# Kernel tuning notes

Measured on AMD Instinct MI355X. Metric: run time of the kernel, lower is better.

Reference implementation:

```python
import jax, jax.numpy as jnp
import numpy as np

DIM, HEADS, DH, M, PINV_ITERS, RES_K = 512, 8, 64, 256, 6, 33

def layernorm(x, w, b, eps=1e-5):
    mu = jnp.mean(x, -1, keepdims=True)
    var = jnp.var(x, -1, keepdims=True)
    return (x - mu) * jax.lax.rsqrt(var + eps) * w + b

def pinv_iter(x, iters=PINV_ITERS):
    # Moore-Penrose iterative pseudo-inverse (lucidrains nystrom-attention)
    ax = jnp.abs(x)
    z = jnp.swapaxes(x, -1, -2) / (jnp.max(ax.sum(-1)) * jnp.max(ax.sum(-2)))
    I = jnp.eye(x.shape[-1], dtype=x.dtype)
    for _ in range(iters):
        xz = x @ z
        z = 0.25 * z @ (13 * I - xz @ (15 * I - xz @ (7 * I - xz)))
    return z

def _core(x, w_qkv):
    b, n, _ = x.shape
    pad = (M - n % M) % M            # Nystrom pads at the FRONT to a multiple of m=256
    xp = jnp.pad(x, ((0, 0), (pad, 0), (0, 0)))
    npad = n + pad
    q, k, v = jnp.split(xp @ w_qkv, 3, axis=-1)
    split_heads = lambda t: t.reshape(b, npad, HEADS, DH).transpose(0, 2, 1, 3)
    q = split_heads(q) * (DH ** -0.5)
    k, v = split_heads(k), split_heads(v)
    l = npad // M                    # tokens per landmark
    q_l = q.reshape(b, HEADS, M, l, DH).mean(3)
    k_l = k.reshape(b, HEADS, M, l, DH).mean(3)
    return q, k, v, q_l, k_l, pad, n

def nystrom_out(x, w_qkv, w_out, b_out, res_kernel):
    q, k, v, q_l, k_l, pad, n = _core(x, w_qkv)
    attn1 = jax.nn.softmax(jnp.einsum('bhid,bhjd->bhij', q, k_l), -1)    # (b,h,N,M)
    attn2 = jax.nn.softmax(jnp.einsum('bhid,bhjd->bhij', q_l, k_l), -1)  # (b,h,M,M)
    attn3 = jax.nn.softmax(jnp.einsum('bhid,bhjd->bhij', q_l, k), -1)    # (b,h,M,N)
    out = (attn1 @ pinv_iter(attn2)) @ (attn3 @ v)
    # depthwise residual conv over sequence dim, per head
    out = out + jax.lax.conv_general_dilated(
        v, res_kernel, (1, 1), [(RES_K // 2, RES_K // 2), (0, 0)],
        dimension_numbers=('NCHW', 'OIHW', 'NCHW'), feature_group_count=HEADS)
    b = out.shape[0]
    out = out.transpose(0, 2, 1, 3).reshape(b, -1, HEADS * DH) @ w_out + b_out
    return out[:, -n:]

def nystrom_cls_row(x, w_qkv):
    # cls-token (query index pad, head 0) row of attn1 @ pinv(attn2) @ attn3;
    # identical math to the full (n x n) matrix row the torch code slices out.
    q, k, v, q_l, k_l, pad, n = _core(x, w_qkv)
    q0, k0, ql0, kl0 = q[:, 0], k[:, 0], q_l[:, 0], k_l[:, 0]
    attn2 = jax.nn.softmax(ql0 @ jnp.swapaxes(kl0, -1, -2), -1)   # (b,M,M)
    attn3 = jax.nn.softmax(ql0 @ jnp.swapaxes(k0, -1, -2), -1)    # (b,M,N)
    row1 = jax.nn.softmax(jnp.einsum('bd,bjd->bj', q0[:, pad], kl0), -1)
    row = jnp.einsum('bj,bjk->bk', row1, pinv_iter(attn2))
    row = jnp.einsum('bk,bkn->bn', row, attn3)                    # (b, N_padded)
    return row, pad

def dwconv(x, k, b, p):
    y = jax.lax.conv_general_dilated(x, k, (1, 1), [(p, p), (p, p)],
        dimension_numbers=('NCHW', 'OIHW', 'NCHW'), feature_group_count=x.shape[1])
    return y + b[None, :, None, None]

def leff(x, k7, b7, k5, b5, k3, b3, Hs, Ws):
    cls_t, feat = x[:, :1], x[:, 1:]
    B, N, C = feat.shape
    img = feat.transpose(0, 2, 1).reshape(B, C, Hs, Ws)
    y = dwconv(img, k7, b7, 3) + img + dwconv(img, k5, b5, 2) + dwconv(img, k3, b3, 1)
    y = y.reshape(B, C, Hs * Ws).transpose(0, 2, 1)
    return jnp.concatenate([cls_t, y], axis=1)

def setup_inputs():
    key = jax.random.key(0)
    ks = iter(jax.random.split(key, 32))
    n, n_classes = 22500, 2
    p = {}
    p['h'] = jax.random.normal(next(ks), (n, 1024), jnp.float32)
    p['fc1_w'] = jax.random.normal(next(ks), (1024, DIM), jnp.float32) * 0.02
    p['fc1_b'] = jnp.zeros((DIM,), jnp.float32)
    p['cls_token'] = jax.random.normal(next(ks), (1, 1, DIM), jnp.float32)
    for pre in ('l1', 'l2'):
        p[pre + '_ln_w'] = jnp.ones((DIM,), jnp.float32)
        p[pre + '_ln_b'] = jnp.zeros((DIM,), jnp.float32)
        p[pre + '_wqkv'] = jax.random.normal(next(ks), (DIM, 3 * HEADS * DH), jnp.float32) * 0.02
        p[pre + '_wout'] = jax.random.normal(next(ks), (HEADS * DH, DIM), jnp.float32) * 0.02
        p[pre + '_bout'] = jnp.zeros((DIM,), jnp.float32)
        p[pre + '_resk'] = jax.random.normal(next(ks), (HEADS, 1, RES_K, 1), jnp.float32) * 0.05
    for kk in (7, 5, 3):
        p['leff_k%d' % kk] = jax.random.normal(next(ks), (DIM, 1, kk, kk), jnp.float32) * 0.05
        p['leff_b%d' % kk] = jnp.zeros((DIM,), jnp.float32)
    p['norm_w'] = jnp.ones((DIM,), jnp.float32)
    p['norm_b'] = jnp.zeros((DIM,), jnp.float32)
    p['fc2_w'] = jax.random.normal(next(ks), (DIM, n_classes), jnp.float32) * 0.02
    p['fc2_b'] = jnp.zeros((n_classes,), jnp.float32)
    return p

def reference(h, fc1_w, fc1_b, cls_token,
              l1_ln_w, l1_ln_b, l1_wqkv, l1_wout, l1_bout, l1_resk,
              leff_k7, leff_b7, leff_k5, leff_b5, leff_k3, leff_b3,
              l2_ln_w, l2_ln_b, l2_wqkv, l2_wout, l2_bout, l2_resk,
              norm_w, norm_b, fc2_w, fc2_b):
    x = h[None]                                   # (1, n, 1024)
    n = x.shape[1]
    x = jax.nn.relu(x @ fc1_w + fc1_b)            # (1, n, 512)
    Hs = int(np.ceil(np.sqrt(n)))                 # 150 for n=22500
    add_len = Hs * Hs - n
    if add_len > 0:
        x = jnp.concatenate([x, x[:, :add_len]], axis=1)
    x = jnp.concatenate([jnp.broadcast_to(cls_token, (1, 1, DIM)), x], axis=1)
    # TransLayer 1
    x = x + nystrom_out(layernorm(x, l1_ln_w, l1_ln_b), l1_wqkv, l1_wout, l1_bout, l1_resk)
    # LeFF positional layer
    x = leff(x, leff_k7, leff_b7, leff_k5, leff_b5, leff_k3, leff_b3, Hs, Hs)
    # TransLayer 2 (first call in TransMIL.forward)
    h2 = x + nystrom_out(layernorm(x, l2_ln_w, l2_ln_b), l2_wqkv, l2_wout, l2_bout, l2_resk)
    # TransLayer 2 second call: residual update then attention matrix of updated state
    h3 = h2 + nystrom_out(layernorm(h2, l2_ln_w, l2_ln_b), l2_wqkv, l2_wout, l2_bout, l2_resk)
    row, pad = nystrom_cls_row(layernorm(h3, l2_ln_w, l2_ln_b), l2_wqkv)
    A = row[0, pad + 1: pad + 1 + n][:, None]     # (n, 1) cls->instance attention
    hf = layernorm(h2, norm_w, norm_b)[:, 0]      # (1, 512)
    logits = hf @ fc2_w + fc2_b                   # (1, n_classes)
    Y_prob = jax.nn.softmax(logits, -1)
    return logits, Y_prob, A
```

## Files before the change

kernel.cpp:

```cpp
#include <hip/hip_runtime.h>

#define NTOK 22500
#define N1   22501
#define NPAD 22528
#define PADR 27
#define DIM  512
#define NH   8
#define DHD  64
#define MM   256
#define LLM  88
#define HSZ  150
#define CSZ  256
#define NCH  88

typedef short bf16x8 __attribute__((ext_vector_type(8)));
typedef float f32x4  __attribute__((ext_vector_type(4)));
typedef unsigned short us;

union U8 { bf16x8 v; unsigned short u[8]; };

__device__ __forceinline__ unsigned short f2b(float f){
  unsigned int u = __float_as_uint(f);
  unsigned int r = u + 0x7fffu + ((u>>16)&1u);
  return (unsigned short)(r>>16);
}
__device__ __forceinline__ float bf2f(unsigned short u){
  return __uint_as_float(((unsigned int)u)<<16);
}
__device__ __forceinline__ bf16x8 cvt8(float4 a, float4 b){
  U8 u;
  u.u[0]=f2b(a.x); u.u[1]=f2b(a.y); u.u[2]=f2b(a.z); u.u[3]=f2b(a.w);
  u.u[4]=f2b(b.x); u.u[5]=f2b(b.y); u.u[6]=f2b(b.z); u.u[7]=f2b(b.w);
  return u.v;
}
__device__ __forceinline__ void gld16(const void* g, void* l){
  __builtin_amdgcn_global_load_lds(
      (const __attribute__((address_space(1))) void*)g,
      (__attribute__((address_space(3))) void*)l, 16, 0, 0);
}

__device__ __forceinline__ float waveSum(float v){
#pragma unroll
  for (int o=32;o>0;o>>=1) v += __shfl_down(v,o);
  return v;
}
__device__ __forceinline__ float waveMax(float v){
#pragma unroll
  for (int o=32;o>0;o>>=1) v = fmaxf(v,__shfl_down(v,o));
  return v;
}
__device__ __forceinline__ float blockSum256(float v, float* sb){
  v = waveSum(v);
  __syncthreads();
  if ((threadIdx.x&63)==0) sb[threadIdx.x>>6]=v;
  __syncthreads();
  return sb[0]+sb[1]+sb[2]+sb[3];
}
__device__ __forceinline__ float blockMax256(float v, float* sb){
  v = waveMax(v);
  __syncthreads();
  if ((threadIdx.x&63)==0) sb[threadIdx.x>>6]=v;
  __syncthreads();
  return fmaxf(fmaxf(sb[0],sb[1]),fmaxf(sb[2],sb[3]));
}

__global__ void k_wT(const float* __restrict__ W, us* __restrict__ Bt, int K, int N)
{
  __shared__ float tile[32][33];
  int tx = threadIdx.x&31, ty = threadIdx.x>>5;
  int k0 = blockIdx.x*32, n0 = blockIdx.y*32;
#pragma unroll
  for (int i=0;i<4;++i){
    int k = k0+ty+i*8;
    if (k<K && n0+tx<N) tile[ty+i*8][tx] = W[(size_t)k*N + n0+tx];
  }
  __syncthreads();
#pragma unroll
  for (int i=0;i<4;++i){
    int n = n0+ty+i*8, k = k0+tx;
    if (n<N && k<K) Bt[(size_t)n*K + k] = f2b(tile[tx][ty+i*8]);
  }
}

__global__ void k_vT(const us* __restrict__ V, us* __restrict__ Vt)
{
  __shared__ us tile[32][33];
  int tx = threadIdx.x&31, ty = threadIdx.x>>5;
  int p0 = blockIdx.x*32;
  int h = blockIdx.y>>1, d0 = (blockIdx.y&1)*32;
#pragma unroll
  for (int i=0;i<4;++i){
    int p = p0+ty+i*8;
    tile[ty+i*8][tx] = V[((size_t)h*NPAD+p)*DHD + d0+tx];
  }
  __syncthreads();
#pragma unroll
  for (int i=0;i<4;++i){
    int d = d0+ty+i*8;
    Vt[((size_t)h*DHD+d)*NPAD + p0+tx] = tile[tx][ty+i*8];
  }
}

template<int MODE, int BM>
__global__ __launch_bounds__(256) void k_gemm(const float* __restrict__ Af,
    const us* __restrict__ Ab, const us* __restrict__ Bt, const float* __restrict__ bias,
    us* __restrict__ Xb, float* __restrict__ Cf, float* __restrict__ C2,
    us* __restrict__ Q_, us* __restrict__ K_, us* __restrict__ V_,
    const us* __restrict__ zpg, int Kd, int ntn)
{
  __shared__ us SM[BM*64 + 128*64];
  us* As = SM;
  us* Bs = SM + BM*64;
  const int tid = threadIdx.x;
  const int bid = blockIdx.x;
  const int ntile = bid % ntn;
  const int m0 = (bid / ntn)*BM, n0 = ntile*128;
  const int lane = tid & 63;
  const int wid = tid >> 6;
  constexpr int MT = BM/32;
  constexpr int ACH = BM/32;
  const int wm = (wid>>1)*(BM/2), wn = (wid&1)*64;
  f32x4 acc[MT][4] = {};
  for (int k0=0; k0<Kd; k0+=64){
    __syncthreads();
    if (MODE==0){
#pragma unroll
      for (int i=0;i<BM/16;++i){
        int g = i*256 + tid;
        int row = g>>4, k4 = (g&15)*4;
        int gm = m0 + row;
        ushort4 h4 = make_ushort4(0,0,0,0);
        if (gm < NTOK){
          float4 v = *(const float4*)(Af + (size_t)gm*Kd + k0 + k4);
          h4.x=f2b(v.x); h4.y=f2b(v.y); h4.z=f2b(v.z); h4.w=f2b(v.w);
        }
        *(ushort4*)(&As[row*64 + (k4 ^ ((row&7)<<3))]) = h4;
      }
    } else {
#pragma unroll
      for (int i=0;i<ACH;++i){
        int c = wid*ACH+i;
        int row = c*8 + (lane>>3);
        int scol8 = ((lane&7) ^ (row&7))*8;
        int gm = m0+row;
        const us* ga;
        if (MODE==2) ga = Ab + ((size_t)((gm<N1?gm:0)+PADR))*Kd + k0 + scol8;
        else ga = (gm>=PADR) ? Ab + (size_t)(gm-PADR)*Kd + k0 + scol8 : zpg + scol8;
        gld16(ga, &As[c*512]);
      }
    }
#pragma unroll
    for (int i=0;i<4;++i){
      int c = wid*4+i;
      int row = c*8 + (lane>>3);
      int scol8 = ((lane&7) ^ (row&7))*8;
      int vn = n0+row;
      if (MODE==3) vn = (vn<64)? vn : vn+448;
      gld16(Bt + (size_t)vn*Kd + k0 + scol8, &Bs[c*512]);
    }
    __syncthreads();
#pragma unroll
    for (int ks=0; ks<2; ++ks){
      const int kk = ks*32 + (lane>>4)*8;
      bf16x8 af[MT], bfm[4];
#pragma unroll
      for (int t=0;t<MT;++t){
        int r = wm + t*16 + (lane&15);
        af[t] = *(bf16x8*)(&As[r*64 + (kk ^ ((r&7)<<3))]);
      }
#pragma unroll
      for (int t=0;t<4;++t){
        int c = wn + t*16 + (lane&15);
        bfm[t] = *(bf16x8*)(&Bs[c*64 + (kk ^ ((c&7)<<3))]);
      }
#pragma unroll
      for (int mt=0;mt<MT;++mt)
#pragma unroll
        for (int nt=0;nt<4;++nt)
          acc[mt][nt] = __builtin_amdgcn_mfma_f32_16x16x32_bf16(af[mt], bfm[nt], acc[mt][nt], 0,0,0);
    }
  }
  const int rbase = (lane>>4)*4;
  const int cl = lane&15;
  if (MODE==3){
#pragma unroll
    for (int mt=0;mt<MT;++mt)
#pragma unroll
      for (int r=0;r<4;++r){
        int gm = m0 + wm + mt*16 + rbase + r;
#pragma unroll
        for (int nt=0;nt<4;++nt){
          int gn = n0 + wn + nt*16 + cl;
          float v = acc[mt][nt][r];
          if (gn < 64) Cf[(size_t)gm*DHD + gn] = v*0.125f;
          else         C2[(size_t)gm*DHD + (gn-64)] = v;
        }
      }
    return;
  }
  const float sc1 = (MODE==1 && (ntile>>2)==0) ? 0.125f : 1.f;
  __syncthreads();
#pragma unroll
  for (int mt=0;mt<MT;++mt)
#pragma unroll
    for (int r=0;r<4;++r){
      int row = wm + mt*16 + rbase + r;
#pragma unroll
      for (int nt=0;nt<4;++nt){
        int col = wn + nt*16 + cl;
        float v = acc[mt][nt][r];
        if (MODE==0){ v += bias[n0+col]; v = v>0.f?v:0.f; }
        else if (MODE==2){ v += bias[n0+col]; }
        else v *= sc1;
        SM[row*128 + col] = f2b(v);
      }
    }
  __syncthreads();
  if (MODE==1){
    const int sec = ntile>>2;
    us* dst = sec==0 ? Q_ : (sec==1 ? K_ : V_);
#pragma unroll
    for (int i=0;i<BM/16;++i){
      int v8 = i*256 + tid;
      int row = v8>>4, c8 = (v8&15)*8;
      int gm = m0 + row, gn = n0 + c8;
      int hh = (gn>>6)&7, d = gn&63;
      *(bf16x8*)(dst + ((size_t)hh*NPAD+gm)*DHD + d) = *(bf16x8*)(&SM[row*128 + c8]);
    }
  } else if (MODE==0){
#pragma unroll
    for (int i=0;i<BM/16;++i){
      int v8 = i*256 + tid;
      int row = v8>>4, c8 = (v8&15)*8;
      int gm = m0 + row;
      if (gm < NTOK)
        *(bf16x8*)(Xb + (size_t)(1+gm)*DIM + n0 + c8) = *(bf16x8*)(&SM[row*128 + c8]);
    }
  } else {
#pragma unroll
    for (int i=0;i<BM/16;++i){
      int v8 = i*256 + tid;
      int row = v8>>4, c8 = (v8&15)*8;
      int gm = m0 + row;
      if (gm < N1){
        us* p = Xb + (size_t)gm*DIM + n0 + c8;
        U8 xo, ad, o;
        xo.v = *(bf16x8*)p;
        ad.v = *(bf16x8*)(&SM[row*128 + c8]);
#pragma unroll
        for (int j=0;j<8;++j) o.u[j] = f2b(bf2f(xo.u[j]) + bf2f(ad.u[j]));
        *(bf16x8*)p = o.v;
      }
    }
  }
}

__global__ void k_setcls(us* __restrict__ X, const float* __restrict__ cls){
  int i = blockIdx.x*256 + threadIdx.x;
  if (i < DIM) X[i] = f2b(cls[i]);
}
__global__ void k_copyu(us* __restrict__ d, const us* __restrict__ s, size_t n){
  size_t i = (size_t)blockIdx.x*256 + threadIdx.x;
  if (i<n) d[i]=s[i];
}

__global__ void k_ln(const us* __restrict__ X, us* __restrict__ Y,
                     const float* __restrict__ w, const float* __restrict__ b)
{
  __shared__ float sb[4];
  const us* x = X + (size_t)blockIdx.x*DIM;
  us* y = Y + (size_t)blockIdx.x*DIM;
  int t = threadIdx.x;
  ushort2 xv = *(const ushort2*)(x + 2*t);
  float a0=bf2f(xv.x), a1=bf2f(xv.y);
  float s = blockSum256(a0+a1, sb);
  float q = blockSum256(a0*a0+a1*a1, sb);
  float mean = s*(1.f/512.f);
  float var = q*(1.f/512.f) - mean*mean;
  float rstd = rsqrtf(var+1e-5f);
  float2 wv = *(const float2*)(w + 2*t);
  float2 bv = *(const float2*)(b + 2*t);
  ushort2 o;
  o.x = f2b((a0-mean)*rstd*wv.x+bv.x);
  o.y = f2b((a1-mean)*rstd*wv.y+bv.y);
  *(ushort2*)(y + 2*t) = o;
}

__global__ void k_landmark2(const us* __restrict__ Q, const us* __restrict__ K,
                            us* __restrict__ QL, us* __restrict__ KL)
{
  int hm = blockIdx.x;
  bool isK = hm >= NH*MM;
  if (isK) hm -= NH*MM;
  int h = hm>>8, m = hm&255; int d = threadIdx.x;
  const us* base = (isK?K:Q) + ((size_t)h*NPAD + (size_t)m*LLM)*DHD + d;
  float s = 0.f;
  for (int j=0;j<LLM;++j) s += bf2f(base[(size_t)j*DHD]);
  (isK?KL:QL)[((size_t)h*MM + m)*DHD + d] = f2b(s * (1.f/(float)LLM));
}
__global__ void k_landmark2f(const float* __restrict__ Q, const float* __restrict__ K,
                             float* __restrict__ QL, float* __restrict__ KL)
{
  int hm = blockIdx.x;
  bool isK = hm >= MM;
  int m = isK ? hm-MM : hm; int d = threadIdx.x;
  const float* base = (isK?K:Q) + (size_t)m*LLM*DHD + d;
  float s = 0.f;
  for (int j=0;j<LLM;++j) s += base[(size_t)j*DHD];
  (isK?KL:QL)[(size_t)m*DHD + d] = s * (1.f/(float)LLM);
}

__global__ __launch_bounds__(64) void k_nt64(const float* __restrict__ A,
    const float* __restrict__ B, float* __restrict__ C,
    long sA, long sB, long sC, int Nr)
{
  int lane = threadIdx.x;
  int n0 = blockIdx.x*64, m0 = blockIdx.y*64;
  A += (size_t)blockIdx.z*sA; B += (size_t)blockIdx.z*sB; C += (size_t)blockIdx.z*sC;
  f32x4 acc[4][4] = {};
#pragma unroll
  for (int ks=0;ks<2;++ks){
    int kk = ks*32 + (lane>>4)*8;
    bf16x8 af[4], bfr[4];
#pragma unroll
    for (int mt=0;mt<4;++mt){
      const float* p = A + (size_t)(m0+mt*16+(lane&15))*64 + kk;
      af[mt] = cvt8(*(const float4*)p, *(const float4*)(p+4));
    }
#pragma unroll
    for (int nt=0;nt<4;++nt){
      const float* p = B + (size_t)(n0+nt*16+(lane&15))*64 + kk;
      bfr[nt] = cvt8(*(const float4*)p, *(const float4*)(p+4));
    }
#pragma unroll
    for (int mt=0;mt<4;++mt)
#pragma unroll
      for (int nt=0;nt<4;++nt)
        acc[mt][nt] = __builtin_amdgcn_mfma_f32_16x16x32_bf16(af[mt], bfr[nt], acc[mt][nt], 0,0,0);
  }
#pragma unroll
  for (int mt=0;mt<4;++mt)
#pragma unroll
    for (int r=0;r<4;++r){
      int row = m0+mt*16+(lane>>4)*4+r;
#pragma unroll
      for (int nt=0;nt<4;++nt){
        int col = n0+nt*16+(lane&15);
        C[(size_t)row*Nr + col] = acc[mt][nt][r];
      }
    }
}

__global__ __launch_bounds__(64) void k_nt64b(const us* __restrict__ A,
    const us* __restrict__ B, float* __restrict__ C,
    long sA, long sB, long sC, int Nr)
{
  int lane = threadIdx.x;
  int n0 = blockIdx.x*64, m0 = blockIdx.y*64;
  A += (size_t)blockIdx.z*sA; B += (size_t)blockIdx.z*sB; C += (size_t)blockIdx.z*sC;
  f32x4 acc[4][4] = {};
#pragma unroll
  for (int ks=0;ks<2;++ks){
    int kk = ks*32 + (lane>>4)*8;
    bf16x8 af[4], bfr[4];
#pragma unroll
    for (int mt=0;mt<4;++mt)
      af[mt] = *(const bf16x8*)(A + (size_t)(m0+mt*16+(lane&15))*64 + kk);
#pragma unroll
    for (int nt=0;nt<4;++nt)
      bfr[nt] = *(const bf16x8*)(B + (size_t)(n0+nt*16+(lane&15))*64 + kk);
#pragma unroll
    for (int mt=0;mt<4;++mt)
#pragma unroll
      for (int nt=0;nt<4;++nt)
        acc[mt][nt] = __builtin_amdgcn_mfma_f32_16x16x32_bf16(af[mt], bfr[nt], acc[mt][nt], 0,0,0);
  }
#pragma unroll
  for (int mt=0;mt<4;++mt)
#pragma unroll
    for (int r=0;r<4;++r){
      int row = m0+mt*16+(lane>>4)*4+r;
#pragma unroll
      for (int nt=0;nt<4;++nt){
        int col = n0+nt*16+(lane&15);
        C[(size_t)row*Nr + col] = acc[mt][nt][r];
      }
    }
}

template<int PM>
__global__ __launch_bounds__(256) void k_pgemm(const us* __restrict__ A,
    const us* __restrict__ Bt, us* __restrict__ C, us* __restrict__ Ct,
    float dc, float alpha, int writeC)
{
  __shared__ us As[64*256];
  __shared__ us Bs[64*256];
  const int tid = threadIdx.x, lane = tid&63, wid = tid>>6;
  const int n0 = blockIdx.x*64, m0 = blockIdx.y*64;
  const us* Ab = A + (size_t)blockIdx.z*65536;
  const us* Bb = Bt + (size_t)blockIdx.z*65536;
  for (int i=tid; i<4096; i+=256){
    int r = i>>6, c4 = (i&63)*4;
    *(ushort4*)(&As[r*256 + (c4 ^ ((r&7)<<3))]) = *(const ushort4*)(Ab + (size_t)(m0+r)*256 + c4);
    *(ushort4*)(&Bs[r*256 + (c4 ^ ((r&7)<<3))]) = *(const ushort4*)(Bb + (size_t)(n0+r)*256 + c4);
  }
  __syncthreads();
  const int wm = (wid>>1)*32, wn = (wid&1)*32;
  f32x4 acc[2][2] = {};
#pragma unroll
  for (int ks=0;ks<8;++ks){
    int kk = ks*32 + (lane>>4)*8;
    bf16x8 af[2], bfr[2];
#pragma unroll
    for (int t=0;t<2;++t){
      int rr = wm + t*16 + (lane&15);
      af[t] = *(const bf16x8*)(&As[rr*256 + (kk ^ ((rr&7)<<3))]);
      int cc = wn + t*16 + (lane&15);
      bfr[t] = *(const bf16x8*)(&Bs[cc*256 + (kk ^ ((cc&7)<<3))]);
    }
#pragma unroll
    for (int mt=0;mt<2;++mt)
#pragma unroll
      for (int nt=0;nt<2;++nt)
        acc[mt][nt] = __builtin_amdgcn_mfma_f32_16x16x32_bf16(af[mt], bfr[nt], acc[mt][nt], 0,0,0);
  }
#pragma unroll
  for (int mt=0;mt<2;++mt)
#pragma unroll
    for (int r=0;r<4;++r){
      int row = m0 + wm + mt*16 + (lane>>4)*4 + r;
#pragma unroll
      for (int nt=0;nt<2;++nt){
        int col = n0 + wn + nt*16 + (lane&15);
        float v = acc[mt][nt][r];
        if (PM==1) v = alpha*(dc*bf2f(Ab[(size_t)row*256+col]) - v);
        us bv = f2b(v);
        if (PM==0 || writeC) C[(size_t)blockIdx.z*65536 + (size_t)row*256 + col] = bv;
        Ct[(size_t)blockIdx.z*65536 + (size_t)col*256 + row] = bv;
      }
    }
}

__global__ __launch_bounds__(256) void k_pgemm2(const us* __restrict__ A,
    const us* __restrict__ Bt, us* __restrict__ Ct)
{
  __shared__ us As[16384];
  __shared__ us Bs[16384];
  const int tid = threadIdx.x, lane = tid&63, wid = tid>>6;
  const int n0 = 0, m0 = blockIdx.y*64;
  const us* Ab = A + (size_t)blockIdx.z*65536;
  const us* Bb = Bt + (size_t)blockIdx.z*16384;
  for (int i=tid; i<4096; i+=256){
    int r = i>>6, c4 = (i&63)*4;
    *(ushort4*)(&As[r*256 + (c4 ^ ((r&7)<<3))]) = *(const ushort4*)(Ab + (size_t)(m0+r)*256 + c4);
    if (r < 64)
      *(ushort4*)(&Bs[r*256 + (c4 ^ ((r&7)<<3))]) = *(const ushort4*)(Bb + (size_t)(n0+r)*256 + c4);
  }
  __syncthreads();
  const int wm = (wid>>1)*32, wn = (wid&1)*32;
  f32x4 acc[2][2] = {};
#pragma unroll
  for (int ks=0;ks<8;++ks){
    int kk = ks*32 + (lane>>4)*8;
    bf16x8 af[2], bfr[2];
#pragma unroll
    for (int t=0;t<2;++t){
      int rr = wm + t*16 + (lane&15);
      af[t] = *(const bf16x8*)(&As[rr*256 + (kk ^ ((rr&7)<<3))]);
      int cc = wn + t*16 + (lane&15);
      bfr[t] = *(const bf16x8*)(&Bs[cc*256 + (kk ^ ((cc&7)<<3))]);
    }
#pragma unroll
    for (int mt=0;mt<2;++mt)
#pragma unroll
      for (int nt=0;nt<2;++nt)
        acc[mt][nt] = __builtin_amdgcn_mfma_f32_16x16x32_bf16(af[mt], bfr[nt], acc[mt][nt], 0,0,0);
  }
#pragma unroll
  for (int mt=0;mt<2;++mt)
#pragma unroll
    for (int r=0;r<4;++r){
      int row = m0 + wm + mt*16 + (lane>>4)*4 + r;
#pragma unroll
      for (int nt=0;nt<2;++nt){
        int col = n0 + wn + nt*16 + (lane&15);
        Ct[(size_t)blockIdx.z*16384 + (size_t)col*256 + row] = f2b(acc[mt][nt][r]);
      }
    }
}

__global__ void k_softmax256(float* __restrict__ S, us* __restrict__ Sb)
{
  __shared__ float sb[4];
  float* row = S + ((size_t)blockIdx.x<<8);
  float x = row[threadIdx.x];
  float m = blockMax256(x, sb);
  float e = __expf(x-m);
  float s = blockSum256(e, sb);
  float p = e/s;
  row[threadIdx.x] = p;
  Sb[((size_t)blockIdx.x<<8) + threadIdx.x] = f2b(p);
}
__global__ void k_csmax(const float* __restrict__ A2, float* __restrict__ sums)
{
  __shared__ float sb[4];
  int b = blockIdx.x, j = threadIdx.x;
  const float* Ab = A2 + ((size_t)b<<16);
  float s = 0.f;
  for (int i=0;i<256;++i) s += Ab[((size_t)i<<8)+j];
  float m = blockMax256(s, sb);
  if (j==0) sums[b] = m;
}
__global__ void k_scale2(const float* __restrict__ sums, float* __restrict__ scl, int nb)
{
  __shared__ float sb[4];
  float m=-1e30f;
  for (int i=threadIdx.x;i<nb;i+=256) m = fmaxf(m, sums[i]);
  m = blockMax256(m, sb);
  if (threadIdx.x==0) scl[0] = 1.f/m;
}
__global__ void k_z0(const float* __restrict__ A2, us* __restrict__ Z, us* __restrict__ Zt,
                     const float* __restrict__ scl)
{
  size_t idx = (size_t)blockIdx.x*256 + threadIdx.x;
  size_t b = idx>>16; int i=(int)((idx>>8)&255), j=(int)(idx&255);
  float v = A2[idx]*scl[0];
  us bv = f2b(v);
  Zt[idx] = bv;
  Z[(b<<16)+((size_t)j<<8)+i] = bv;
}

__global__ __launch_bounds__(256) void k_attn3(const us* __restrict__ QLb,
    const us* __restrict__ Kb, const us* __restrict__ Vt,
    float* __restrict__ Pmax, float* __restrict__ Psum, us* __restrict__ Pacc)
{
  __shared__ us Ks[64*64];
  __shared__ us Vs[64*64];
  __shared__ us Ps[4*64*64];
  int h = blockIdx.y, cx = blockIdx.x;
  int tid = threadIdx.x, wid = tid>>6, lane = tid&63;
  bf16x8 aq[4][2];
#pragma unroll
  for (int mt=0;mt<4;++mt){
    const us* qp = QLb + ((size_t)h*MM + wid*64 + mt*16 + (lane&15))*DHD;
#pragma unroll
    for (int ks=0;ks<2;++ks)
      aq[mt][ks] = *(const bf16x8*)(qp + ks*32 + (lane>>4)*8);
  }
  float m_[4][4], l_[4][4];
  f32x4 acc[4][4] = {};
#pragma unroll
  for (int mt=0;mt<4;++mt)
#pragma unroll
    for (int r=0;r<4;++r){ m_[mt][r] = -1e30f; l_[mt][r] = 0.f; }

  us* Pw = &Ps[wid*4096];
  for (int t=0;t<4;++t){
    int kb0 = cx*CSZ + t*64;
    __syncthreads();
    for (int i=tid;i<1024;i+=256){
      int rr = i>>4, c4 = (i&15)*4;
      ushort4 ku = *(const ushort4*)(Kb + ((size_t)h*NPAD + kb0 + rr)*DHD + c4);
      *(ushort4*)(&Ks[rr*64 + (c4 ^ ((rr&7)<<3))]) = ku;
      ushort4 vu = *(const ushort4*)(Vt + ((size_t)h*DHD + rr)*NPAD + kb0 + c4);
      *(ushort4*)(&Vs[rr*64 + (c4 ^ ((rr&7)<<3))]) = vu;
    }
    __syncthreads();
    f32x4 s[4][4] = {};
#pragma unroll
    for (int ks=0;ks<2;++ks){
      int kk = ks*32 + (lane>>4)*8;
      bf16x8 kbf[4];
#pragma unroll
      for (int nt=0;nt<4;++nt){
        int key = nt*16 + (lane&15);
        kbf[nt] = *(const bf16x8*)(&Ks[key*64 + (kk ^ ((key&7)<<3))]);
      }
#pragma unroll
      for (int mt=0;mt<4;++mt)
#pragma unroll
        for (int nt=0;nt<4;++nt)
          s[mt][nt] = __builtin_amdgcn_mfma_f32_16x16x32_bf16(aq[mt][ks], kbf[nt], s[mt][nt], 0,0,0);
    }
#pragma unroll
    for (int mt=0;mt<4;++mt){
#pragma unroll
      for (int r=0;r<4;++r){
        float mx = fmaxf(fmaxf(s[mt][0][r], s[mt][1][r]), fmaxf(s[mt][2][r], s[mt][3][r]));
#pragma unroll
        for (int off=8;off>=1;off>>=1) mx = fmaxf(mx, __shfl_xor(mx, off));
        float mn = fmaxf(m_[mt][r], mx);
        float f = __expf(m_[mt][r]-mn);
        float la = 0.f;
#pragma unroll
        for (int nt=0;nt<4;++nt){ float p=__expf(s[mt][nt][r]-mn); s[mt][nt][r]=p; la+=p; }
#pragma unroll
        for (int off=8;off>=1;off>>=1) la += __shfl_xor(la, off);
        l_[mt][r] = l_[mt][r]*f + la;
        m_[mt][r] = mn;
#pragma unroll
        for (int dt=0;dt<4;++dt) acc[mt][dt][r] *= f;
      }
    }
#pragma unroll
    for (int mt=0;mt<4;++mt)
#pragma unroll
      for (int r=0;r<4;++r){
        int row = mt*16 + (lane>>4)*4 + r;
        int sw = (row&7)<<3;
#pragma unroll
        for (int nt=0;nt<4;++nt){
          int col = nt*16 + (lane&15);
          Pw[row*64 + (col ^ sw)] = f2b(s[mt][nt][r]);
        }
      }
#pragma unroll
    for (int ks=0;ks<2;++ks){
      int kk = ks*32 + (lane>>4)*8;
      bf16x8 pa[4], vb[4];
#pragma unroll
      for (int mt=0;mt<4;++mt){
        int arow = mt*16 + (lane&15);
        pa[mt] = *(const bf16x8*)(&Pw[arow*64 + (kk ^ ((arow&7)<<3))]);
      }
#pragma unroll
      for (int dt=0;dt<4;++dt){
        int d = dt*16 + (lane&15);
        vb[dt] = *(const bf16x8*)(&Vs[d*64 + (kk ^ ((d&7)<<3))]);
      }
#pragma unroll
      for (int mt=0;mt<4;++mt)
#pragma unroll
        for (int dt=0;dt<4;++dt)
          acc[mt][dt] = __builtin_amdgcn_mfma_f32_16x16x32_bf16(pa[mt], vb[dt], acc[mt][dt], 0,0,0);
    }
  }
  size_t pbase = ((size_t)h*NCH + cx)*MM;
#pragma unroll
  for (int mt=0;mt<4;++mt)
#pragma unroll
    for (int r=0;r<4;++r){
      int row = wid*64 + mt*16 + (lane>>4)*4 + r;
      if ((lane&15)==0){ Pmax[pbase+row]=m_[mt][r]; Psum[pbase+row]=l_[mt][r]; }
#pragma unroll
      for (int dt=0;dt<4;++dt)
        Pacc[(pbase+row)*DHD + dt*16+(lane&15)] = f2b(acc[mt][dt][r]);
    }
}

__global__ void k_attn3_merge(const float* __restrict__ Pmax, const float* __restrict__ Psum,
    const us* __restrict__ Pacc, us* __restrict__ A3Vtb)
{
  int hm = blockIdx.x; int h = hm>>8, m = hm&255; int d = threadIdx.x;
  float gm = -1e30f;
  for (int c=0;c<NCH;++c) gm = fmaxf(gm, Pmax[((size_t)h*NCH+c)*MM+m]);
  float tot=0.f, acc=0.f;
  for (int c=0;c<NCH;++c){
    size_t pi = ((size_t)h*NCH+c)*MM+m;
    float w = __expf(Pmax[pi]-gm);
    tot += Psum[pi]*w;
    acc += bf2f(Pacc[pi*DHD+d])*w;
  }
  A3Vtb[((size_t)h*DHD + d)*MM + m] = f2b(acc/tot);
}

__global__ __launch_bounds__(256) void k_attn1(const us* __restrict__ Qb,
    const us* __restrict__ KLb, const us* __restrict__ WmT,
    us* __restrict__ OH)
{
  __shared__ us KWs[64*256];
  __shared__ us Ps[64*256];
  int h = blockIdx.y, tid = threadIdx.x;
  int wid = tid>>6, lane = tid&63;
  int q0 = blockIdx.x*64;
  for (int i=tid; i<4096; i+=256){
    int lm = i>>4, k4 = (i&15)*4;
    *(ushort4*)(&KWs[lm*64 + (k4 ^ ((lm&7)<<3))]) =
        *(const ushort4*)(KLb + ((size_t)h*MM + lm)*DHD + k4);
  }
  bf16x8 aq[2];
  const us* qp = Qb + ((size_t)h*NPAD + q0 + wid*16 + (lane&15))*DHD;
#pragma unroll
  for (int ks=0;ks<2;++ks)
    aq[ks] = *(const bf16x8*)(qp + ks*32 + (lane>>4)*8);
  __syncthreads();
  f32x4 s[16];
#pragma unroll
  for (int nt=0;nt<16;++nt) s[nt] = (f32x4){0.f,0.f,0.f,0.f};
#pragma unroll
  for (int ks=0;ks<2;++ks){
    int kk = ks*32 + (lane>>4)*8;
#pragma unroll
    for (int nt=0;nt<16;++nt){
      int col = nt*16 + (lane&15);
      bf16x8 b = *(const bf16x8*)(&KWs[col*64 + (kk ^ ((col&7)<<3))]);
      s[nt] = __builtin_amdgcn_mfma_f32_16x16x32_bf16(aq[ks], b, s[nt], 0,0,0);
    }
  }
  float rcp[4];
#pragma unroll
  for (int r=0;r<4;++r){
    float m = -1e30f;
#pragma unroll
    for (int nt=0;nt<16;++nt) m = fmaxf(m, s[nt][r]);
#pragma unroll
    for (int off=8;off>=1;off>>=1) m = fmaxf(m, __shfl_xor(m, off));
    float l = 0.f;
#pragma unroll
    for (int nt=0;nt<16;++nt){ float p=__expf(s[nt][r]-m); s[nt][r]=p; l+=p; }
#pragma unroll
    for (int off=8;off>=1;off>>=1) l += __shfl_xor(l, off);
    rcp[r] = 1.f/l;
  }
  int prow_base = wid*16 + (lane>>4)*4;
#pragma unroll
  for (int nt=0;nt<16;++nt){
    int col = nt*16 + (lane&15);
#pragma unroll
    for (int r=0;r<4;++r){
      int row = prow_base + r;
      Ps[row*256 + (col ^ ((row&7)<<3))] = f2b(s[nt][r]);
    }
  }
  __syncthreads();
  for (int i=tid; i<4096; i+=256){
    int d = i>>6, k4 = (i&63)*4;
    ushort4 u = *(const ushort4*)(WmT + ((size_t)h*DHD + d)*MM + k4);
    *(ushort4*)(&KWs[d*256 + (k4 ^ ((d&7)<<3))]) = u;
  }
  __syncthreads();
  f32x4 acc[4] = {};
  int arow = wid*16 + (lane&15);
#pragma unroll
  for (int ks=0;ks<8;++ks){
    int kk = ks*32 + (lane>>4)*8;
    bf16x8 a = *(const bf16x8*)(&Ps[arow*256 + (kk ^ ((arow&7)<<3))]);
#pragma unroll
    for (int dt=0;dt<4;++dt){
      int d = dt*16 + (lane&15);
      bf16x8 b = *(const bf16x8*)(&KWs[d*256 + (kk ^ ((d&7)<<3))]);
      acc[dt] = __builtin_amdgcn_mfma_f32_16x16x32_bf16(a, b, acc[dt], 0,0,0);
    }
  }
#pragma unroll
  for (int r=0;r<4;++r){
    int row = q0 + prow_base + r;
    us* op = OH + (size_t)row*DIM + h*DHD;
#pragma unroll
    for (int dt=0;dt<4;++dt)
      op[dt*16 + (lane&15)] = f2b(acc[dt][r]*rcp[r]);
  }
}

#define SCBLK 32
__global__ __launch_bounds__(256) void k_seqconv(const us* __restrict__ Vb,
    const float* __restrict__ resk, us* __restrict__ OH)
{
  __shared__ us Vs[64*512];
  int tid = threadIdx.x;
  int p0 = blockIdx.x*SCBLK;
  for (int i=tid; i<16384; i+=256){
    int pl = i>>8, c2 = i&255;
    int gp = p0 - 16 + pl;
    int hh = c2>>5, d2 = (c2&31)*2;
    ushort2 v = make_ushort2(0,0);
    if (gp>=0 && gp<NPAD) v = *(const ushort2*)(Vb + ((size_t)hh*NPAD+gp)*DHD + d2);
    *(ushort2*)(&Vs[pl*512 + c2*2]) = v;
  }
  __syncthreads();
  int h = tid>>5;
  float kr[33];
#pragma unroll
  for (int r=0;r<33;++r) kr[r] = resk[h*33+r];
  for (int pl=0; pl<SCBLK; ++pl){
    float s0=0.f, s1=0.f;
#pragma unroll
    for (int r=0;r<33;++r){
      ushort2 v = *(const ushort2*)(&Vs[(pl+r)*512 + tid*2]);
      s0 += bf2f(v.x)*kr[r];
      s1 += bf2f(v.y)*kr[r];
    }
    size_t o = (size_t)(p0+pl)*DIM + tid*2;
    ushort2 cur = *(ushort2*)(OH + o);
    *(ushort2*)(OH + o) = make_ushort2(f2b(bf2f(cur.x)+s0), f2b(bf2f(cur.y)+s1));
  }
}

__global__ void k_tfwd(const us* __restrict__ X, us* __restrict__ T)
{
  __shared__ us tile[32][33];
  int tx = threadIdx.x & 31, ty = threadIdx.x >> 5;
  int s0 = blockIdx.x*32, c0 = blockIdx.y*32;
  for (int yy=0; yy<4; ++yy){
    int s = s0 + ty + yy*8;
    if (s < NTOK) tile[ty+yy*8][tx] = X[(size_t)(1+s)*DIM + c0+tx];
  }
  __syncthreads();
  for (int yy=0; yy<4; ++yy){
    int c = c0 + ty + yy*8;
    int s = s0 + tx;
    if (s < NTOK) T[(size_t)c*NTOK + s] = tile[tx][ty+yy*8];
  }
}
__global__ void k_tbwd(const us* __restrict__ T, us* __restrict__ X)
{
  __shared__ us tile[32][33];
  int tx = threadIdx.x & 31, ty = threadIdx.x >> 5;
  int s0 = blockIdx.x*32, c0 = blockIdx.y*32;
  for (int yy=0; yy<4; ++yy){
    int c = c0 + ty + yy*8, s = s0 + tx;
    if (s < NTOK) tile[ty+yy*8][tx] = T[(size_t)c*NTOK + s];
  }
  __syncthreads();
  for (int yy=0; yy<4; ++yy){
    int s = s0 + ty + yy*8, c = c0 + tx;
    if (s < NTOK) X[(size_t)(1+s)*DIM + c] = tile[tx][ty+yy*8];
  }
}
__global__ __launch_bounds__(256) void k_leff(const us* __restrict__ T,
    const float* __restrict__ k7, const float* __restrict__ b7,
    const float* __restrict__ k5, const float* __restrict__ b5,
    const float* __restrict__ k3, const float* __restrict__ b3,
    us* __restrict__ T2)
{
  __shared__ float tile[21*21];
  int c = blockIdx.y;
  int ti = blockIdx.x/10, tj = blockIdx.x%10;
  int i0 = ti*15-3, j0 = tj*15-3;
  const us* img = T + (size_t)c*NTOK;
  for (int idx=threadIdx.x; idx<441; idx+=256){
    int ii = idx/21, jj = idx%21;
    int gi = i0+ii, gj = j0+jj;
    tile[idx] = (gi>=0 && gi<HSZ && gj>=0 && gj<HSZ) ? bf2f(img[gi*HSZ+gj]) : 0.f;
  }
  __syncthreads();
  if (threadIdx.x < 225){
    int li = threadIdx.x/15, lj = threadIdx.x%15;
    int gi = ti*15+li, gj = tj*15+lj;
    float acc = tile[(li+3)*21 + (lj+3)] + b7[c]+b5[c]+b3[c];
    const float* w7 = k7 + c*49;
#pragma unroll
    for (int a=0;a<7;++a)
#pragma unroll
      for (int bb=0;bb<7;++bb) acc += tile[(li+a)*21 + (lj+bb)]*w7[a*7+bb];
    const float* w5 = k5 + c*25;
#pragma unroll
    for (int a=0;a<5;++a)
#pragma unroll
      for (int bb=0;bb<5;++bb) acc += tile[(li+1+a)*21 + (lj+1+bb)]*w5[a*5+bb];
    const float* w3 = k3 + c*9;
#pragma unroll
    for (int a=0;a<3;++a)
#pragma unroll
      for (int bb=0;bb<3;++bb) acc += tile[(li+2+a)*21 + (lj+2+bb)]*w3[a*3+bb];
    T2[(size_t)c*NTOK + gi*HSZ+gj] = f2b(acc);
  }
}

__global__ void k_row1(const float* __restrict__ Q0, const float* __restrict__ KL0,
                       float* __restrict__ row1)
{
  __shared__ float sb[4];
  __shared__ float qv[64];
  int t = threadIdx.x;
  if (t<64) qv[t] = Q0[PADR*DHD + t];
  __syncthreads();
  float l = 0.f;
#pragma unroll
  for (int d=0;d<64;++d) l += qv[d]*KL0[(size_t)t*DHD+d];
  float m = blockMax256(l, sb);
  float e = __expf(l-m);
  float s = blockSum256(e, sb);
  row1[t] = e/s;
}
__global__ void k_rz(const float* __restrict__ row1, const us* __restrict__ Zt,
                     float* __restrict__ rz)
{
  __shared__ float r1[256];
  int t = threadIdx.x;
  r1[t] = row1[t];
  __syncthreads();
  float s = 0.f;
  for (int k2=0;k2<256;++k2) s += r1[k2]*bf2f(Zt[(size_t)t*MM + k2]);
  rz[t] = s;
}
__global__ void k_rowstat(const float* __restrict__ L0, float* __restrict__ mx, float* __restrict__ se)
{
  __shared__ float sb[4];
  const float* row = L0 + (size_t)blockIdx.x*NPAD;
  float m = -1e30f;
  for (int i=threadIdx.x;i<NPAD;i+=256) m = fmaxf(m, row[i]);
  m = blockMax256(m, sb);
  float s = 0.f;
  for (int i=threadIdx.x;i<NPAD;i+=256) s += __expf(row[i]-m);
  s = blockSum256(s, sb);
  if (threadIdx.x==0){ mx[blockIdx.x]=m; se[blockIdx.x]=s; }
}
__global__ void k_aout(const float* __restrict__ L0, const float* __restrict__ rz,
    const float* __restrict__ mx, const float* __restrict__ se, float* __restrict__ out)
{
  __shared__ float wk[256], mk[256];
  int t = threadIdx.x;
  wk[t] = rz[t]/se[t];
  mk[t] = mx[t];
  __syncthreads();
  int p = blockIdx.x*256 + t;
  if (p >= NTOK) return;
  size_t pp = (size_t)(PADR+1+p);
  float a = 0.f;
  for (int k2=0;k2<256;++k2) a += wk[k2]*__expf(L0[(size_t)k2*NPAD+pp]-mk[k2]);
  out[4+p] = a;
}
__global__ void k_final(const us* __restrict__ H2r, const float* __restrict__ nw,
    const float* __restrict__ nbb, const float* __restrict__ w2, const float* __restrict__ b2,
    float* __restrict__ out)
{
  __shared__ float sb[4];
  __shared__ float hf[512];
  int t = threadIdx.x;
  float x0 = bf2f(H2r[t]), x1 = bf2f(H2r[256+t]);
  float s = blockSum256(x0+x1, sb);
  float q = blockSum256(x0*x0+x1*x1, sb);
  float mean = s*(1.f/512.f);
  float var = q*(1.f/512.f) - mean*mean;
  float rstd = rsqrtf(var+1e-5f);
  hf[t]     = (x0-mean)*rstd*nw[t]+nbb[t];
  hf[256+t] = (x1-mean)*rstd*nw[256+t]+nbb[256+t];
  __syncthreads();
  float p0 = hf[t]*w2[t*2]   + hf[256+t]*w2[(256+t)*2];
  float p1 = hf[t]*w2[t*2+1] + hf[256+t]*w2[(256+t)*2+1];
  p0 = blockSum256(p0, sb);
  p1 = blockSum256(p1, sb);
  if (t==0){
    float l0 = p0+b2[0], l1 = p1+b2[1];
    float m = fmaxf(l0,l1);
    float e0 = __expf(l0-m), e1 = __expf(l1-m), si = 1.f/(e0+e1);
    out[0]=l0; out[1]=l1; out[2]=e0*si; out[3]=e1*si;
  }
}

struct Bufs {
  float *A2,*sums,*scl,*Pmax,*Psum;
  us *Xb,*Yb,*OHb,*Qb,*Kb,*Vb,*Vtb,*QLb,*KLb,*A2b;
  us *Z0b,*Z0tb,*Z1b,*Z1tb,*XZb,*XZtb,*T1tb,*T2tb;
  us *A3Vtb,*WmT,*Pacc,*zpg;
};

static void run_pinv(const us* A2b, Bufs& b, int NB, hipStream_t st)
{
  dim3 g(4,4,NB);
  us *Zc=b.Z0b, *Zct=b.Z0tb, *Zn=b.Z1b, *Znt=b.Z1tb;
  for (int it=0; it<6; ++it){
    k_pgemm<0><<<g,256,0,st>>>(A2b, Zct, b.XZb, b.XZtb, 0.f, 1.f, 1);
    k_pgemm<1><<<g,256,0,st>>>(b.XZb, b.XZtb, nullptr, b.T1tb, 7.f, 1.f, 0);
    k_pgemm<1><<<g,256,0,st>>>(b.XZb, b.T1tb, nullptr, b.T2tb, 15.f, 1.f, 0);
    k_pgemm<1><<<g,256,0,st>>>(Zc, b.T2tb, Zn, Znt, 13.f, 0.25f, 1);
    us* t1=Zc; Zc=Zn; Zn=t1;
    us* t2=Zct; Zct=Znt; Znt=t2;
  }
}

static void nystrom_layer(Bufs& b, const float* lnw, const float* lnb,
    const us* wqkvT, const us* woutT,
    const float* bout, const float* resk, hipStream_t st)
{
  k_ln<<<N1,256,0,st>>>(b.Xb, b.Yb, lnw, lnb);
  k_gemm<1,128><<<176*12,256,0,st>>>(nullptr, b.Yb, wqkvT, nullptr,
      nullptr, nullptr, nullptr, b.Qb, b.Kb, b.Vb, b.zpg, DIM, 12);
  k_vT<<<dim3(NPAD/32,16),256,0,st>>>(b.Vb, b.Vtb);
  k_landmark2<<<2*NH*MM,64,0,st>>>(b.Qb, b.Kb, b.QLb, b.KLb);
  k_nt64b<<<dim3(4,4,NH),64,0,st>>>(b.QLb, b.KLb, b.A2,
      (long)MM*DHD,(long)MM*DHD,(long)MM*MM, MM);
  k_softmax256<<<NH*MM,256,0,st>>>(b.A2, b.A2b);
  k_csmax<<<NH,256,0,st>>>(b.A2, b.sums);
  k_scale2<<<1,256,0,st>>>(b.sums, b.scl, NH);
  k_z0<<<NH*MM*MM/256,256,0,st>>>(b.A2, b.Z0b, b.Z0tb, b.scl);
  run_pinv(b.A2b, b, NH, st);
  k_attn3<<<dim3(NCH,NH),256,0,st>>>(b.QLb, b.Kb, b.Vtb, b.Pmax, b.Psum, b.Pacc);
  k_attn3_merge<<<NH*MM,64,0,st>>>(b.Pmax, b.Psum, b.Pacc, b.A3Vtb);
  k_pgemm2<<<dim3(1,4,NH),256,0,st>>>(b.Z0b, b.A3Vtb, b.WmT);
  k_attn1<<<dim3(NPAD/64,NH),256,0,st>>>(b.Qb, b.KLb, b.WmT, b.OHb);
  k_seqconv<<<NPAD/SCBLK,256,0,st>>>(b.Vb, resk, b.OHb);
  k_gemm<2,64><<<352*4,256,0,st>>>(nullptr, b.OHb, woutT, bout,
      b.Xb, nullptr, nullptr, nullptr, nullptr, nullptr, b.zpg, DIM, 4);
}

extern "C" void kernel_launch(void* const* d_in, const int* in_sizes, int n_in,
                              void* d_out, int out_size, void* d_ws, size_t ws_size,
                              hipStream_t stream)
{
  (void)n_in; (void)out_size;
  bool sig_order = (in_sizes[10] == 25088);
  int iL2 = sig_order ? 16 : 10;
  int iLf = sig_order ? 10 : 16;

  const float* h       = (const float*)d_in[0];
  const float* fc1_w   = (const float*)d_in[1];
  const float* fc1_b   = (const float*)d_in[2];
  const float* cls_tok = (const float*)d_in[3];
  const float* l1_lnw  = (const float*)d_in[4];
  const float* l1_lnb  = (const float*)d_in[5];
  const float* l1_wqkv = (const float*)d_in[6];
  const float* l1_wout = (const float*)d_in[7];
  const float* l1_bout = (const float*)d_in[8];
  const float* l1_resk = (const float*)d_in[9];
  const float* l2_lnw  = (const float*)d_in[iL2+0];
  const float* l2_lnb  = (const float*)d_in[iL2+1];
  const float* l2_wqkv = (const float*)d_in[iL2+2];
  const float* l2_wout = (const float*)d_in[iL2+3];
  const float* l2_bout = (const float*)d_in[iL2+4];
  const float* l2_resk = (const float*)d_in[iL2+5];
  const float* k7 = (const float*)d_in[iLf+0];
  const float* b7 = (const float*)d_in[iLf+1];
  const float* k5 = (const float*)d_in[iLf+2];
  const float* b5 = (const float*)d_in[iLf+3];
  const float* k3 = (const float*)d_in[iLf+4];
  const float* b3 = (const float*)d_in[iLf+5];
  const float* nw = (const float*)d_in[22];
  const float* nbb= (const float*)d_in[23];
  const float* w2 = (const float*)d_in[24];
  const float* b2 = (const float*)d_in[25];
  float* out = (float*)d_out;

  char* base = (char*)d_ws;
  auto allocF = [&](size_t n)->float*{
    float* p=(float*)base; base += ((n*sizeof(float)+255)&~(size_t)255); return p; };
  auto allocU = [&](size_t n)->us*{
    us* p=(us*)base; base += ((n*sizeof(us)+255)&~(size_t)255); return p; };

  const size_t S = (size_t)NPAD*DIM;
  const size_t SQ = (size_t)MM*MM;
  Bufs b;
  b.Xb  = allocU(S);
  b.Yb  = allocU(S);
  b.OHb = allocU(S);
  b.Qb  = allocU(S);
  b.Kb  = allocU(S);
  b.Vb  = allocU(S);
  b.Vtb = allocU(S);
  b.QLb = allocU((size_t)NH*MM*DHD);
  b.KLb = allocU((size_t)NH*MM*DHD);
  b.A2  = allocF((size_t)NH*SQ);
  b.A2b = allocU((size_t)NH*SQ);
  b.Z0b = allocU((size_t)NH*SQ);  b.Z0tb = allocU((size_t)NH*SQ);
  b.Z1b = allocU((size_t)NH*SQ);  b.Z1tb = allocU((size_t)NH*SQ);
  b.XZb = allocU((size_t)NH*SQ);  b.XZtb = allocU((size_t)NH*SQ);
  b.T1tb= allocU((size_t)NH*SQ);
  b.T2tb= allocU((size_t)NH*SQ);
  b.A3Vtb = allocU((size_t)NH*MM*DHD);
  b.WmT   = allocU((size_t)NH*MM*DHD);
  b.sums  = allocF(2*(size_t)NH*MM);
  b.scl   = allocF(16);
  b.Pmax  = allocF((size_t)NH*NCH*MM);
  b.Psum  = allocF((size_t)NH*NCH*MM);
  b.Pacc  = allocU((size_t)NH*NCH*MM*DHD);
  b.zpg   = allocU(512);
  us* fc1T   = allocU((size_t)DIM*1024);
  us* wqkvT1 = allocU((size_t)1536*DIM);
  us* wqkvT2 = allocU((size_t)1536*DIM);
  us* woutT1 = allocU((size_t)DIM*DIM);
  us* woutT2 = allocU((size_t)DIM*DIM);
  float* Q0   = allocF((size_t)NPAD*DHD);
  float* K0   = allocF((size_t)NPAD*DHD);
  float* QL0f = allocF((size_t)MM*DHD);
  float* KL0f = allocF((size_t)MM*DHD);
  float* row1 = allocF(256);
  float* rzv  = allocF(256);
  float* mxv  = allocF(256);
  float* sev  = allocF(256);
  us* h2row = allocU(512);
  if ((size_t)(base - (char*)d_ws) > ws_size) return;

  hipMemsetAsync((void*)b.zpg, 0, 1024, stream);

  k_wT<<<dim3(32,16),256,0,stream>>>(fc1_w, fc1T, 1024, DIM);
  k_wT<<<dim3(16,48),256,0,stream>>>(l1_wqkv, wqkvT1, DIM, 1536);
  k_wT<<<dim3(16,48),256,0,stream>>>(l2_wqkv, wqkvT2, DIM, 1536);
  k_wT<<<dim3(16,16),256,0,stream>>>(l1_wout, woutT1, DIM, DIM);
  k_wT<<<dim3(16,16),256,0,stream>>>(l2_wout, woutT2, DIM, DIM);

  k_gemm<0,64><<<352*4,256,0,stream>>>(h, nullptr, fc1T, fc1_b,
      b.Xb, nullptr, nullptr, nullptr, nullptr, nullptr, b.zpg, 1024, 4);
  k_setcls<<<2,256,0,stream>>>(b.Xb, cls_tok);

  nystrom_layer(b, l1_lnw, l1_lnb, wqkvT1, woutT1, l1_bout, l1_resk, stream);
  k_tfwd<<<dim3(704,16),256,0,stream>>>(b.Xb, b.OHb);
  k_leff<<<dim3(100,512),256,0,stream>>>(b.OHb, k7,b7,k5,b5,k3,b3, b.Qb);
  k_tbwd<<<dim3(704,16),256,0,stream>>>(b.Qb, b.Xb);

  nystrom_layer(b, l2_lnw, l2_lnb, wqkvT2, woutT2, l2_bout, l2_resk, stream);
  k_copyu<<<2,256,0,stream>>>(h2row, b.Xb, 512);

  nystrom_layer(b, l2_lnw, l2_lnb, wqkvT2, woutT2, l2_bout, l2_resk, stream);

  k_ln<<<N1,256,0,stream>>>(b.Xb, b.Yb, l2_lnw, l2_lnb);
  k_gemm<3,64><<<352,256,0,stream>>>(nullptr, b.Yb, wqkvT2, nullptr,
      nullptr, Q0, K0, nullptr, nullptr, nullptr, b.zpg, DIM, 1);
  k_landmark2f<<<2*MM,64,0,stream>>>(Q0, K0, QL0f, KL0f);
  k_nt64<<<dim3(4,4,1),64,0,stream>>>(QL0f, KL0f, b.A2, 0,0,0, MM);
  k_softmax256<<<MM,256,0,stream>>>(b.A2, b.A2b);
  k_csmax<<<1,256,0,stream>>>(b.A2, b.sums);
  k_scale2<<<1,256,0,stream>>>(b.sums, b.scl, 1);
  k_z0<<<MM*MM/256,256,0,stream>>>(b.A2, b.Z0b, b.Z0tb, b.scl);
  run_pinv(b.A2b, b, 1, stream);
  k_row1<<<1,256,0,stream>>>(Q0, KL0f, row1);
  k_rz<<<1,256,0,stream>>>(row1, b.Z0tb, rzv);
  float* L0 = (float*)b.Yb;
  k_nt64<<<dim3(NPAD/64,4,1),64,0,stream>>>(QL0f, K0, L0, 0,0,0, NPAD);
  k_rowstat<<<MM,256,0,stream>>>(L0, mxv, sev);
  k_aout<<<88,256,0,stream>>>(L0, rzv, mxv, sev, out);
  k_final<<<1,256,0,stream>>>(h2row, nw, nbb, w2, b2, out);
}
```

Baseline: 2.492 ms.

## Coalesce pinv GEMM epilogue via LDS transpose, reorder GEMM tiles, tile z0 transpose

The pinv GEMM epilogue now stages the output tile in swizzled shared memory. Both the row-major and transposed outputs are then written with 16-byte vector stores, replacing scattered 2-byte stores. The dc*A term is read from the already-loaded shared A tile instead of global memory. The main GEMM block index now iterates M fastest (N tile = bid/mtn), changing which blocks share weight tiles in cache. The z0 init uses a shared-memory tiled transpose for coalesced writes.

After: 2.355 ms. -5.5%, faster.

```diff
diff --git a/kernel.cpp b/kernel.cpp
--- a/kernel.cpp
+++ b/kernel.cpp
@@ -106,15 +106,15 @@
     const us* __restrict__ Ab, const us* __restrict__ Bt, const float* __restrict__ bias,
     us* __restrict__ Xb, float* __restrict__ Cf, float* __restrict__ C2,
     us* __restrict__ Q_, us* __restrict__ K_, us* __restrict__ V_,
-    const us* __restrict__ zpg, int Kd, int ntn)
+    const us* __restrict__ zpg, int Kd, int mtn)
 {
   __shared__ us SM[BM*64 + 128*64];
   us* As = SM;
   us* Bs = SM + BM*64;
   const int tid = threadIdx.x;
   const int bid = blockIdx.x;
-  const int ntile = bid % ntn;
-  const int m0 = (bid / ntn)*BM, n0 = ntile*128;
+  const int ntile = bid / mtn;
+  const int m0 = (bid % mtn)*BM, n0 = ntile*128;
   const int lane = tid & 63;
   const int wid = tid >> 6;
   constexpr int MT = BM/32;
@@ -424,21 +424,56 @@
       for (int nt=0;nt<2;++nt)
         acc[mt][nt] = __builtin_amdgcn_mfma_f32_16x16x32_bf16(af[mt], bfr[nt], acc[mt][nt], 0,0,0);
   }
+  float vv[2][4][2];
 #pragma unroll
   for (int mt=0;mt<2;++mt)
 #pragma unroll
-    for (int r=0;r<4;++r){
-      int row = m0 + wm + mt*16 + (lane>>4)*4 + r;
+    for (int q=0;q<4;++q){
+      int rl = wm + mt*16 + (lane>>4)*4 + q;
 #pragma unroll
       for (int nt=0;nt<2;++nt){
-        int col = n0 + wn + nt*16 + (lane&15);
-        float v = acc[mt][nt][r];
-        if (PM==1) v = alpha*(dc*bf2f(Ab[(size_t)row*256+col]) - v);
-        us bv = f2b(v);
-        if (PM==0 || writeC) C[(size_t)blockIdx.z*65536 + (size_t)row*256 + col] = bv;
-        Ct[(size_t)blockIdx.z*65536 + (size_t)col*256 + row] = bv;
-      }
-    }
+        int clx = wn + nt*16 + (lane&15);
+        float v = acc[mt][nt][q];
+        if (PM==1) v = alpha*(dc*bf2f(As[rl*256 + (clx ^ ((rl&7)<<3))]) - v);
+        vv[mt][q][nt] = v;
+      }
+    }
+  __syncthreads();
+  us* TT = As;
+#pragma unroll
+  for (int mt=0;mt<2;++mt)
+#pragma unroll
+    for (int q=0;q<4;++q){
+      int rl = wm + mt*16 + (lane>>4)*4 + q;
+      int sw = (rl&7)<<3;
+#pragma unroll
+      for (int nt=0;nt<2;++nt){
+        int clx = wn + nt*16 + (lane&15);
+        TT[rl*64 + (clx ^ sw)] = f2b(vv[mt][q][nt]);
+      }
+    }
+  __syncthreads();
+  {
+    int c = tid>>2, r0 = (tid&3)*16;
+    U8 b0, b1;
+#pragma unroll
+    for (int i=0;i<8;++i){
+      int r = r0+i;       b0.u[i] = TT[r*64 + (c ^ ((r&7)<<3))];
+      int r2 = r0+8+i;    b1.u[i] = TT[r2*64 + (c ^ ((r2&7)<<3))];
+    }
+    us* dst = Ct + (size_t)blockIdx.z*65536 + (size_t)(n0+c)*256 + m0 + r0;
+    *(bf16x8*)dst = b0.v;
+    *(bf16x8*)(dst+8) = b1.v;
+  }
+  if (PM==0 || writeC){
+    int rr = tid>>2, c0 = (tid&3)*16;
+    int sw = (rr&7)<<3;
+    bf16x8 x0 = *(const bf16x8*)(&TT[rr*64 + (c0 ^ sw)]);
+    bf16x8 x1 = *(const bf16x8*)(&TT[rr*64 + ((c0+8) ^ sw)]);
+    us* dc2 = C + (size_t)blockIdx.z*65536 + (size_t)(m0+rr)*256 + n0 + c0;
+    *(bf16x8*)dc2 = x0;
+    *(bf16x8*)(dc2+8) = x1;
+  }
 }
 
 __global__ __launch_bounds__(256) void k_pgemm2(const us* __restrict__ A,
@@ -519,15 +554,30 @@
   m = blockMax256(m, sb);
   if (threadIdx.x==0) scl[0] = 1.f/m;
 }
-__global__ void k_z0(const float* __restrict__ A2, us* __restrict__ Z, us* __restrict__ Zt,
-                     const float* __restrict__ scl)
-{
-  size_t idx = (size_t)blockIdx.x*256 + threadIdx.x;
-  size_t b = idx>>16; int i=(int)((idx>>8)&255), j=(int)(idx&255);
-  float v = A2[idx]*scl[0];
-  us bv = f2b(v);
-  Zt[idx] = bv;
-  Z[(b<<16)+((size_t)j<<8)+i] = bv;
+__global__ void k_z0t(const float* __restrict__ A2, us* __restrict__ Z, us* __restrict__ Zt,
+                      const float* __restrict__ scl)
+{
+  __shared__ us tile[32][33];
+  int tx = threadIdx.x&31, ty = threadIdx.x>>5;
+  int i0 = blockIdx.x*32;
+  int head = blockIdx.y>>3, j0 = (blockIdx.y&7)*32;
+  float s = scl[0];
+  const float* Ab = A2 + (size_t)head*65536;
+  us* Zh  = Z  + (size_t)head*65536;
+  us* Zth = Zt + (size_t)head*65536;
+#pragma unroll
+  for (int ii=0;ii<4;++ii){
+    int i = i0+ty+ii*8;
+    us bv = f2b(Ab[(size_t)i*256 + j0+tx]*s);
+    Zth[(size_t)i*256 + j0+tx] = bv;
+    tile[ty+ii*8][tx] = bv;
+  }
+  __syncthreads();
+#pragma unroll
+  for (int ii=0;ii<4;++ii){
+    int j = j0+ty+ii*8;
+    Zh[(size_t)j*256 + i0+tx] = tile[tx][ty+ii*8];
+  }
 }
 
 __global__ __launch_bounds__(256) void k_attn3(const us* __restrict__ QLb,
@@ -966,7 +1016,7 @@
 {
   k_ln<<<N1,256,0,st>>>(b.Xb, b.Yb, lnw, lnb);
   k_gemm<1,128><<<176*12,256,0,st>>>(nullptr, b.Yb, wqkvT, nullptr,
-      nullptr, nullptr, nullptr, b.Qb, b.Kb, b.Vb, b.zpg, DIM, 12);
+      nullptr, nullptr, nullptr, b.Qb, b.Kb, b.Vb, b.zpg, DIM, 176);
   k_vT<<<dim3(NPAD/32,16),256,0,st>>>(b.Vb, b.Vtb);
   k_landmark2<<<2*NH*MM,64,0,st>>>(b.Qb, b.Kb, b.QLb, b.KLb);
   k_nt64b<<<dim3(4,4,NH),64,0,st>>>(b.QLb, b.KLb, b.A2,
@@ -974,7 +1024,7 @@
   k_softmax256<<<NH*MM,256,0,st>>>(b.A2, b.A2b);
   k_csmax<<<NH,256,0,st>>>(b.A2, b.sums);
   k_scale2<<<1,256,0,st>>>(b.sums, b.scl, NH);
-  k_z0<<<NH*MM*MM/256,256,0,st>>>(b.A2, b.Z0b, b.Z0tb, b.scl);
+  k_z0t<<<dim3(8,8*NH),256,0,st>>>(b.A2, b.Z0b, b.Z0tb, b.scl);
   run_pinv(b.A2b, b, NH, st);
   k_attn3<<<dim3(NCH,NH),256,0,st>>>(b.QLb, b.Kb, b.Vtb, b.Pmax, b.Psum, b.Pacc);
   k_attn3_merge<<<NH*MM,64,0,st>>>(b.Pmax, b.Psum, b.Pacc, b.A3Vtb);
@@ -982,7 +1032,7 @@
   k_attn1<<<dim3(NPAD/64,NH),256,0,st>>>(b.Qb, b.KLb, b.WmT, b.OHb);
   k_seqconv<<<NPAD/SCBLK,256,0,st>>>(b.Vb, resk, b.OHb);
   k_gemm<2,64><<<352*4,256,0,st>>>(nullptr, b.OHb, woutT, bout,
-      b.Xb, nullptr, nullptr, nullptr, nullptr, nullptr, b.zpg, DIM, 4);
+      b.Xb, nullptr, nullptr, nullptr, nullptr, nullptr, b.zpg, DIM, 352);
 }
 
 extern "C" void kernel_launch(void* const* d_in, const int* in_sizes, int n_in,
@@ -1080,7 +1130,7 @@
   k_wT<<<dim3(16,16),256,0,stream>>>(l2_wout, woutT2, DIM, DIM);
 
   k_gemm<0,64><<<352*4,256,0,stream>>>(h, nullptr, fc1T, fc1_b,
-      b.Xb, nullptr, nullptr, nullptr, nullptr, nullptr, b.zpg, 1024, 4);
+      b.Xb, nullptr, nullptr, nullptr, nullptr, nullptr, b.zpg, 1024, 352);
   k_setcls<<<2,256,0,stream>>>(b.Xb, cls_tok);
 
   nystrom_layer(b, l1_lnw, l1_lnb, wqkvT1, woutT1, l1_bout, l1_resk, stream);
@@ -1095,13 +1145,13 @@
 
   k_ln<<<N1,256,0,stream>>>(b.Xb, b.Yb, l2_lnw, l2_lnb);
   k_gemm<3,64><<<352,256,0,stream>>>(nullptr, b.Yb, wqkvT2, nullptr,
-      nullptr, Q0, K0, nullptr, nullptr, nullptr, b.zpg, DIM, 1);
+      nullptr, Q0, K0, nullptr, nullptr, nullptr, b.zpg, DIM, 352);
   k_landmark2f<<<2*MM,64,0,stream>>>(Q0, K0, QL0f, KL0f);
   k_nt64<<<dim3(4,4,1),64,0,stream>>>(QL0f, KL0f, b.A2, 0,0,0, MM);
   k_softmax256<<<MM,256,0,stream>>>(b.A2, b.A2b);
   k_csmax<<<1,256,0,stream>>>(b.A2, b.sums);
   k_scale2<<<1,256,0,stream>>>(b.sums, b.scl, 1);
-  k_z0<<<MM*MM/256,256,0,stream>>>(b.A2, b.Z0b, b.Z0tb, b.scl);
+  k_z0t<<<dim3(8,8),256,0,stream>>>(b.A2, b.Z0b, b.Z0tb, b.scl);
   run_pinv(b.A2b, b, 1, stream);
   k_row1<<<1,256,0,stream>>>(Q0, KL0f, row1);
   k_rz<<<1,256,0,stream>>>(row1, b.Z0tb, rzv);
```
